# Performance work log

Hardware: AMD Instinct MI355X
Metric: run time of the kernel (lower is better)

## Reference

```python
import jax, jax.numpy as jnp
import numpy as np


def _conv3d(x, w, b, pad_t):
    # x: (b, c, t, h, w); w: (out_c, in_c, kt, 1, 1); conv only along time dim
    y = jax.lax.conv_general_dilated(
        x, w, window_strides=(1, 1, 1),
        padding=((pad_t, pad_t), (0, 0), (0, 0)),
        dimension_numbers=('NCDHW', 'OIDHW', 'NCDHW'))
    return y + b[None, :, None, None, None]


def setup_inputs() -> dict:
    key = jax.random.key(0)
    ks = jax.random.split(key, 8)
    b, t, c, h, w = 4, 16, 64, 96, 96
    cq = c // 8
    s = 0.05
    return {
        'x': jax.random.normal(ks[0], (b, t, c, h, w), jnp.float32),
        'wq': jax.random.normal(ks[1], (cq, c, 3, 1, 1), jnp.float32) * s,
        'bq': jax.random.normal(ks[2], (cq,), jnp.float32) * s,
        'wk': jax.random.normal(ks[3], (cq, c, 3, 1, 1), jnp.float32) * s,
        'bk': jax.random.normal(ks[4], (cq,), jnp.float32) * s,
        'wv': jax.random.normal(ks[5], (c, c, 1, 1, 1), jnp.float32) * s,
        'bv': jax.random.normal(ks[6], (c,), jnp.float32) * s,
        'gamma': jax.random.normal(ks[7], (1,), jnp.float32) * 0.1,
    }


def reference(x, wq, bq, wk, bk, wv, bv, gamma):
    b, t, c, h, w = x.shape
    xc = jnp.transpose(x, (0, 2, 1, 3, 4))  # (b, c, t, h, w)
    # q, k: (b, t, c//8 * h * w); v: (b, t, c * h * w)
    q = jnp.transpose(_conv3d(xc, wq, bq, 1), (0, 2, 1, 3, 4)).reshape(b, t, -1)
    k = jnp.transpose(_conv3d(xc, wk, bk, 1), (0, 2, 1, 3, 4)).reshape(b, t, -1)
    v = jnp.transpose(_conv3d(xc, wv, bv, 0), (0, 2, 1, 3, 4)).reshape(b, t, -1)
    energy = jnp.einsum('btd,bsd->bts', q, k)          # (b, t, t)
    heat = jax.nn.softmax(energy, axis=-1)             # softmax over dim 2
    out = jnp.einsum('bts,bsd->btd', heat, v).reshape(b, t, c, h, w)
    return gamma * out + x
```

## Files before the change

### kernel.cpp

```cpp
#include <hip/hip_runtime.h>
#include <math.h>

#define B_  4
#define T_  16
#define C_  64
#define CQ_ 8
#define HW_ 9216
#define NCH_ 576

typedef __attribute__((ext_vector_type(8))) short    s16x8;
typedef __attribute__((ext_vector_type(4))) float    f32x4;
typedef __attribute__((ext_vector_type(4))) unsigned u32x4;

static __device__ __forceinline__ short f2bf(float f) {
  union { float f; unsigned u; } v; v.f = f;
  return (short)((v.u + 0x7FFFu + ((v.u >> 16) & 1u)) >> 16);
}
static __device__ __forceinline__ unsigned pkbf(float lo, float hi) {
  unsigned r;
  asm("v_cvt_pk_bf16_f32 %0, %1, %2" : "=v"(r) : "v"(lo), "v"(hi));
  return r;
}
static __device__ __forceinline__ float ubf(unsigned u) {
  union { unsigned u; float f; } v; v.u = u; return v.f;
}

__global__ __launch_bounds__(256)
void k_prep(const float* __restrict__ wq, const float* __restrict__ wk,
            const float* __restrict__ wv, short* __restrict__ wqkb,
            short* __restrict__ wvb) {
  for (int idx = threadIdx.x; idx < 3072; idx += 256) {
    int j = idx & 7, lane = (idx >> 3) & 63, ks = idx >> 9;
    int m = lane & 15, lq = lane >> 4;
    int ci = (ks & 1) * 32 + lq * 8 + j;
    int d  = ks >> 1;
    float wval = (m < 8) ? wq[(m * C_ + ci) * 3 + d]
                         : wk[((m - 8) * C_ + ci) * 3 + d];
    wqkb[idx] = f2bf(wval);
  }
  for (int idx = threadIdx.x; idx < 4096; idx += 256) {
    int j = idx & 7, lane = (idx >> 3) & 63, fr = idx >> 9;
    int ct = fr >> 1, ks = fr & 1;
    int c  = ct * 16 + (lane & 15);
    int ci = ks * 32 + (lane >> 4) * 8 + j;
    wvb[idx] = f2bf(wv[c * C_ + ci]);
  }
}

__global__ __launch_bounds__(512, 4)
void k_energy(const float* __restrict__ x, const short* __restrict__ wqkb,
              const float* __restrict__ bq, const float* __restrict__ bk,
              float* __restrict__ partE) {
  __shared__ __attribute__((aligned(16))) short sh[29440];
  __shared__ float Ered[1024];

  const int b    = blockIdx.y;
  const int hw0  = blockIdx.x * 16;
  const int tid  = threadIdx.x;
  const int lane = tid & 63, w = tid >> 6;
  const int l15  = lane & 15, lq = lane >> 4;
  const f32x4 fz = {0.f, 0.f, 0.f, 0.f};

  for (int i = tid; i < 1152; i += 512)
    ((unsigned*)sh)[(i < 576) ? i : (9216 + i)] = 0;

  s16x8 afr[6];
#pragma unroll
  for (int ks = 0; ks < 6; ++ks)
    afr[ks] = *(const s16x8*)&wqkb[(ks * 64 + lane) * 8];

  const float* bias = (lq < 2) ? bq : bk;
  const int cqb = (lq & 1) * 4;
  const float b0 = bias[cqb + 0], b1 = bias[cqb + 1];
  const float b2 = bias[cqb + 2], b3 = bias[cqb + 3];

  {
    const int q4 = tid & 3;
    const int cp = (tid >> 2) & 31;
    const int s0 = tid >> 7;
    const float* xb = x + (size_t)(b * T_ * C_ + 2 * cp) * HW_ + hw0 + 4 * q4;
#pragma unroll
    for (int it = 0; it < 4; ++it) {
      const int s = s0 * 4 + it;
      float4 v0 = *(const float4*)(xb + (size_t)(s * C_) * HW_);
      float4 v1 = *(const float4*)(xb + (size_t)(s * C_) * HW_ + HW_);
      const int off = ((cp >> 2) ^ ((s + 1) & 7)) * 8 + 2 * (cp & 3);
      const int rb  = (s + 1) * 16 + 4 * q4;
      *(unsigned*)&sh[(rb + 0) * 72 + off] = pkbf(v0.x, v1.x);
      *(unsigned*)&sh[(rb + 1) * 72 + off] = pkbf(v0.y, v1.y);
      *(unsigned*)&sh[(rb + 2) * 72 + off] = pkbf(v0.z, v1.z);
      *(unsigned*)&sh[(rb + 3) * 72 + off] = pkbf(v0.w, v1.w);
    }
  }
  __syncthreads();

#pragma unroll
  for (int gl = 0; gl < 2; ++gl) {
    const int g = w * 2 + gl;
    f32x4 a = fz;
#pragma unroll
    for (int ks = 0; ks < 6; ++ks) {
      const int d = ks >> 1;
      const int row = (l15 + d) * 16 + g;
      const int chunk = (((ks & 1) * 4 + lq) ^ ((l15 + d) & 7));
      s16x8 bf = *(const s16x8*)&sh[row * 72 + chunk * 8];
      a = __builtin_amdgcn_mfma_f32_16x16x32_bf16(afr[ks], bf, a, 0, 0, 0);
    }
    const float v0 = a[0] + b0, v1 = a[1] + b1;
    const float v2 = a[2] + b2, v3 = a[3] + b3;
    const unsigned h01 = pkbf(v0, v1), h23 = pkbf(v2, v3);
    const unsigned l01 = pkbf(v0 - ubf(h01 << 16), v1 - ubf(h01 & 0xffff0000u));
    const unsigned l23 = pkbf(v2 - ubf(h23 << 16), v3 - ubf(h23 & 0xffff0000u));
    short* pl = &sh[20736 + (lq >> 1) * 4352 + l15 * 136 + g * 8 + (lq & 1) * 4];
    uint2 hh; hh.x = h01; hh.y = h23;
    uint2 ll; ll.x = l01; ll.y = l23;
    *(uint2*)pl          = hh;
    *(uint2*)(pl + 2176) = ll;
  }
  __syncthreads();

  if (w < 4) {
    const int off = l15 * 136 + w * 32 + lq * 8;
    const short* Qp = &sh[20736];
    const short* Kp = &sh[20736 + 4352];
    s16x8 qh = *(const s16x8*)&Qp[off];
    s16x8 ql = *(const s16x8*)&Qp[off + 2176];
    s16x8 kh = *(const s16x8*)&Kp[off];
    s16x8 kl = *(const s16x8*)&Kp[off + 2176];
    f32x4 e = fz;
    e = __builtin_amdgcn_mfma_f32_16x16x32_bf16(qh, kh, e, 0, 0, 0);
    e = __builtin_amdgcn_mfma_f32_16x16x32_bf16(qh, kl, e, 0, 0, 0);
    e = __builtin_amdgcn_mfma_f32_16x16x32_bf16(ql, kh, e, 0, 0, 0);
#pragma unroll
    for (int r = 0; r < 4; ++r)
      Ered[w * 256 + (lq * 4 + r) * 16 + l15] = e[r];
  }
  __syncthreads();

  if (tid < 256) {
    float e = Ered[tid] + Ered[256 + tid] + Ered[512 + tid] + Ered[768 + tid];
    partE[((size_t)(b * NCH_ + blockIdx.x)) * 256 + tid] = e;
  }
}

__global__ __launch_bounds__(256)
void k_softmax(const float* __restrict__ partE, float* __restrict__ heat) {
  const int b = blockIdx.x;
  const int tid = threadIdx.x;
  float e = 0.f;
  for (int ch = 0; ch < NCH_; ++ch)
    e += partE[((size_t)(b * NCH_ + ch)) * 256 + tid];
  float mx = e;
#pragma unroll
  for (int m = 1; m < 16; m <<= 1) mx = fmaxf(mx, __shfl_xor(mx, m, 64));
  float ex = expf(e - mx);
  float sm = ex;
#pragma unroll
  for (int m = 1; m < 16; m <<= 1) sm += __shfl_xor(sm, m, 64);
  heat[b * 256 + tid] = ex / sm;
}

__global__ __launch_bounds__(256, 3)
void k_mix(const float* __restrict__ x, const float* __restrict__ heat,
           const short* __restrict__ wvb, const float* __restrict__ bv,
           const float* __restrict__ gam, float* __restrict__ out) {
  __shared__ __attribute__((aligned(16))) short sm[20480];

  const int b    = blockIdx.y;
  const int hw0  = blockIdx.x * 16;
  const int tid  = threadIdx.x;
  const int lane = tid & 63;
  const int w    = tid >> 6;
  const int l15  = lane & 15;
  const int lq   = lane >> 4;

  union U8 { s16x8 v; int i[4]; unsigned u[4]; };
  const f32x4 fz = {0.f, 0.f, 0.f, 0.f};

  U8 ha; ha.i[0] = ha.i[1] = ha.i[2] = ha.i[3] = 0;
  if (lane < 32) {
    const float* hp = heat + b * 256 + l15 * 16 + lq * 8;
    float4 h0 = *(const float4*)hp;
    float4 h1 = *(const float4*)(hp + 4);
    ha.u[0] = pkbf(h0.x, h0.y); ha.u[1] = pkbf(h0.z, h0.w);
    ha.u[2] = pkbf(h1.x, h1.y); ha.u[3] = pkbf(h1.z, h1.w);
  }

  {
    const int ci = tid >> 2, q = tid & 3;
    const int sx = ci & 7;
    const float* xp = x + ((size_t)b * T_ * C_ + ci) * HW_ + hw0 + q * 4;
    short* r0 = &sm[(ci * 16 + q * 4) * 20];
#pragma unroll
    for (int P = 0; P < 8; ++P) {
      float4 v0 = *(const float4*)(xp + (size_t)(2 * P) * C_ * HW_);
      float4 v1 = *(const float4*)(xp + (size_t)(2 * P + 1) * C_ * HW_);
      const int ip = (P ^ sx) * 2;
      *(unsigned*)&r0[ip]      = pkbf(v0.x, v1.x);
      *(unsigned*)&r0[20 + ip] = pkbf(v0.y, v1.y);
      *(unsigned*)&r0[40 + ip] = pkbf(v0.z, v1.z);
      *(unsigned*)&r0[60 + ip] = pkbf(v0.w, v1.w);
    }
  }

  U8 a2[8];
#pragma unroll
  for (int fr = 0; fr < 8; ++fr)
    a2[fr].v = *(const s16x8*)&wvb[(fr * 64 + lane) * 8];

  asm volatile("s_waitcnt lgkmcnt(0)" ::: "memory");

  const int lq2 = lq & 1;
  f32x4 c1[16];
#pragma unroll
  for (int i = 0; i < 16; ++i) {
    const int ci = w * 16 + i;
    const short* row = &sm[(ci * 16 + l15) * 20];
    const int base = (lq2 * 4) ^ (i & 4);
    int2 D0 = *(const int2*)&row[2 * base];
    int2 D1 = *(const int2*)&row[2 * base + 4];
    U8 bx;
    const int t3 = i & 3;
    bx.i[0] = (t3 == 0) ? D0.x : (t3 == 1) ? D0.y : (t3 == 2) ? D1.x : D1.y;
    bx.i[1] = (t3 == 0) ? D0.y : (t3 == 1) ? D0.x : (t3 == 2) ? D1.y : D1.x;
    bx.i[2] = (t3 == 0) ? D1.x : (t3 == 1) ? D1.y : (t3 == 2) ? D0.x : D0.y;
    bx.i[3] = (t3 == 0) ? D1.y : (t3 == 1) ? D1.x : (t3 == 2) ? D0.y : D0.x;
    c1[i] = __builtin_amdgcn_mfma_f32_16x16x32_bf16(ha.v, bx.v, fz, 0, 0, 0);
  }
  __syncthreads();

  unsigned rc[32];
#pragma unroll
  for (int ct = 0; ct < 4; ++ct)
#pragma unroll
    for (int r = 0; r < 4; ++r) {
      const int c = ct * 16 + lq * 4 + r;
      const short* row = &sm[(c * 16 + l15) * 20];
      const int base = 4 * ((w >> 1) ^ (lq & 1)) + 2 * ((w & 1) ^ (r >> 1));
      int2 D = *(const int2*)&row[2 * base];
      rc[(ct * 4 + r) * 2 + 0] = (r & 1) ? (unsigned)D.y : (unsigned)D.x;
      rc[(ct * 4 + r) * 2 + 1] = (r & 1) ? (unsigned)D.x : (unsigned)D.y;
    }
  __syncthreads();

#pragma unroll
  for (int r = 0; r < 4; ++r) {
    const int t = lq * 4 + r;
    short* dst = &sm[(t * 16 + l15) * 72 + w * 16];
    u32x4 p0, p1;
    p0[0] = pkbf(c1[0][r],  c1[1][r]);  p0[1] = pkbf(c1[2][r],  c1[3][r]);
    p0[2] = pkbf(c1[4][r],  c1[5][r]);  p0[3] = pkbf(c1[6][r],  c1[7][r]);
    p1[0] = pkbf(c1[8][r],  c1[9][r]);  p1[1] = pkbf(c1[10][r], c1[11][r]);
    p1[2] = pkbf(c1[12][r], c1[13][r]); p1[3] = pkbf(c1[14][r], c1[15][r]);
    *(u32x4*)dst       = p0;
    *(u32x4*)(dst + 8) = p1;
  }

  f32x4 bvr[4];
#pragma unroll
  for (int ct = 0; ct < 4; ++ct)
    bvr[ct] = *(const f32x4*)(bv + ct * 16 + lq * 4);
  const float gamma = gam[0];
  __syncthreads();

#pragma unroll
  for (int ntq = 0; ntq < 4; ++ntq) {
    const int t = w * 4 + ntq;
    const short* xr0 = &sm[(t * 16 + l15) * 72];
    s16x8 b0 = *(const s16x8*)(xr0 + lq * 8);
    s16x8 b1 = *(const s16x8*)(xr0 + 32 + lq * 8);
    float* op = out + ((size_t)(b * T_ + t) * C_) * HW_ + hw0 + l15;
    const int half = ntq >> 1, odd = ntq & 1;
#pragma unroll
    for (int ct = 0; ct < 4; ++ct) {
      f32x4 acc = __builtin_amdgcn_mfma_f32_16x16x32_bf16(a2[ct * 2 + 0].v, b0, fz, 0, 0, 0);
      acc = __builtin_amdgcn_mfma_f32_16x16x32_bf16(a2[ct * 2 + 1].v, b1, acc, 0, 0, 0);
      const int cb = ct * 16 + lq * 4;
#pragma unroll
      for (int r = 0; r < 4; ++r) {
        const unsigned v = rc[(ct * 4 + r) * 2 + half];
        union { unsigned u; float f; } z;
        z.u = odd ? (v & 0xffff0000u) : (v << 16);
        __builtin_nontemporal_store(
            gamma * (acc[r] + bvr[ct][r]) + z.f,
            &op[(size_t)(cb + r) * HW_]);
      }
    }
  }
}

extern "C" void kernel_launch(void* const* d_in, const int* in_sizes, int n_in,
                              void* d_out, int out_size, void* d_ws, size_t ws_size,
                              hipStream_t stream) {
  const float* x   = (const float*)d_in[0];
  const float* wq  = (const float*)d_in[1];
  const float* bq  = (const float*)d_in[2];
  const float* wk  = (const float*)d_in[3];
  const float* bk  = (const float*)d_in[4];
  const float* wv  = (const float*)d_in[5];
  const float* bv  = (const float*)d_in[6];
  const float* gam = (const float*)d_in[7];
  float* out = (float*)d_out;

  short* wqkb  = (short*)d_ws;
  short* wvb   = wqkb + 3072;
  float* partE = (float*)(wvb + 4096 + 1024);
  float* heat  = partE + (size_t)B_ * NCH_ * 256;

  k_prep   <<<1, 256, 0, stream>>>(wq, wk, wv, wqkb, wvb);
  k_energy <<<dim3(NCH_, B_), 512, 0, stream>>>(x, wqkb, bq, bk, partE);
  k_softmax<<<dim3(B_),       256, 0, stream>>>(partE, heat);
  k_mix    <<<dim3(HW_ / 16, B_), 256, 0, stream>>>(x, heat, wvb, bv, gam, out);
}
```

Baseline: 148.2 us.

## Widen softmax reduction to 1024 threads and double k_mix tile to 32 pixels

The softmax kernel now splits the 576-chunk partial-energy sum across four thread groups and combines them through shared memory, which shortens the serial reduction loop per thread. The mix kernel now handles 32 spatial positions per block with 512 threads (two 16-pixel halves across eight waves), doubling shared memory and halving the grid. This is meant to amortize weight and heat loads and per-block overhead. The cost is fewer blocks and higher LDS use per block, which may reduce occupancy.

```diff
diff --git a/kernel.cpp b/kernel.cpp
--- a/kernel.cpp
+++ b/kernel.cpp
@@ -143,34 +143,43 @@
   }
 }
 
-__global__ __launch_bounds__(256)
+__global__ __launch_bounds__(1024)
 void k_softmax(const float* __restrict__ partE, float* __restrict__ heat) {
+  __shared__ float red[1024];
   const int b = blockIdx.x;
   const int tid = threadIdx.x;
-  float e = 0.f;
-  for (int ch = 0; ch < NCH_; ++ch)
-    e += partE[((size_t)(b * NCH_ + ch)) * 256 + tid];
-  float mx = e;
-#pragma unroll
-  for (int m = 1; m < 16; m <<= 1) mx = fmaxf(mx, __shfl_xor(mx, m, 64));
-  float ex = expf(e - mx);
-  float sm = ex;
-#pragma unroll
-  for (int m = 1; m < 16; m <<= 1) sm += __shfl_xor(sm, m, 64);
-  heat[b * 256 + tid] = ex / sm;
-}
-
-__global__ __launch_bounds__(256, 3)
+  const int e = tid & 255, z = tid >> 8;
+  float s = 0.f;
+  for (int ch = z; ch < NCH_; ch += 4)
+    s += partE[((size_t)(b * NCH_ + ch)) * 256 + e];
+  red[tid] = s;
+  __syncthreads();
+  if (z == 0) {
+    float ev = red[e] + red[256 + e] + red[512 + e] + red[768 + e];
+    float mx = ev;
+#pragma unroll
+    for (int m = 1; m < 16; m <<= 1) mx = fmaxf(mx, __shfl_xor(mx, m, 64));
+    float ex = expf(ev - mx);
+    float sm = ex;
+#pragma unroll
+    for (int m = 1; m < 16; m <<= 1) sm += __shfl_xor(sm, m, 64);
+    heat[b * 256 + e] = ex / sm;
+  }
+}
+
+__global__ __launch_bounds__(512, 2)
 void k_mix(const float* __restrict__ x, const float* __restrict__ heat,
            const short* __restrict__ wvb, const float* __restrict__ bv,
            const float* __restrict__ gam, float* __restrict__ out) {
-  __shared__ __attribute__((aligned(16))) short sm[20480];
+  __shared__ __attribute__((aligned(16))) short sm[40960];
 
   const int b    = blockIdx.y;
-  const int hw0  = blockIdx.x * 16;
+  const int hw0  = blockIdx.x * 32;
   const int tid  = threadIdx.x;
   const int lane = tid & 63;
   const int w    = tid >> 6;
+  const int wg   = w & 3;
+  const int gh   = w >> 2;
   const int l15  = lane & 15;
   const int lq   = lane >> 4;
 
@@ -187,10 +196,11 @@
   }
 
   {
-    const int ci = tid >> 2, q = tid & 3;
-    const int sx = ci & 7;
-    const float* xp = x + ((size_t)b * T_ * C_ + ci) * HW_ + hw0 + q * 4;
-    short* r0 = &sm[(ci * 16 + q * 4) * 20];
+    const int ciS = wg * 16 + (lane >> 2);
+    const int gS  = gh * 16 + (lane & 3) * 4;
+    const int sx  = ciS & 7;
+    const float* xp = x + ((size_t)b * T_ * C_ + ciS) * HW_ + hw0 + gS;
+    short* r0 = &sm[(ciS * 32 + gS) * 20];
 #pragma unroll
     for (int P = 0; P < 8; ++P) {
       float4 v0 = *(const float4*)(xp + (size_t)(2 * P) * C_ * HW_);
@@ -214,8 +224,8 @@
   f32x4 c1[16];
 #pragma unroll
   for (int i = 0; i < 16; ++i) {
-    const int ci = w * 16 + i;
-    const short* row = &sm[(ci * 16 + l15) * 20];
+    const int ci = wg * 16 + i;
+    const short* row = &sm[(ci * 32 + gh * 16 + l15) * 20];
     const int base = (lq2 * 4) ^ (i & 4);
     int2 D0 = *(const int2*)&row[2 * base];
     int2 D1 = *(const int2*)&row[2 * base + 4];
@@ -235,8 +245,8 @@
 #pragma unroll
     for (int r = 0; r < 4; ++r) {
       const int c = ct * 16 + lq * 4 + r;
-      const short* row = &sm[(c * 16 + l15) * 20];
-      const int base = 4 * ((w >> 1) ^ (lq & 1)) + 2 * ((w & 1) ^ (r >> 1));
+      const short* row = &sm[(c * 32 + gh * 16 + l15) * 20];
+      const int base = 4 * ((wg >> 1) ^ (lq & 1)) + 2 * ((wg & 1) ^ (r >> 1));
       int2 D = *(const int2*)&row[2 * base];
       rc[(ct * 4 + r) * 2 + 0] = (r & 1) ? (unsigned)D.y : (unsigned)D.x;
       rc[(ct * 4 + r) * 2 + 1] = (r & 1) ? (unsigned)D.x : (unsigned)D.y;
@@ -246,7 +256,7 @@
 #pragma unroll
   for (int r = 0; r < 4; ++r) {
     const int t = lq * 4 + r;
-    short* dst = &sm[(t * 16 + l15) * 72 + w * 16];
+    short* dst = &sm[(t * 32 + gh * 16 + l15) * 72 + wg * 16];
     u32x4 p0, p1;
     p0[0] = pkbf(c1[0][r],  c1[1][r]);  p0[1] = pkbf(c1[2][r],  c1[3][r]);
     p0[2] = pkbf(c1[4][r],  c1[5][r]);  p0[3] = pkbf(c1[6][r],  c1[7][r]);
@@ -265,11 +275,11 @@
 
 #pragma unroll
   for (int ntq = 0; ntq < 4; ++ntq) {
-    const int t = w * 4 + ntq;
-    const short* xr0 = &sm[(t * 16 + l15) * 72];
+    const int t = wg * 4 + ntq;
+    const short* xr0 = &sm[(t * 32 + gh * 16 + l15) * 72];
     s16x8 b0 = *(const s16x8*)(xr0 + lq * 8);
     s16x8 b1 = *(const s16x8*)(xr0 + 32 + lq * 8);
-    float* op = out + ((size_t)(b * T_ + t) * C_) * HW_ + hw0 + l15;
+    float* op = out + ((size_t)(b * T_ + t) * C_) * HW_ + hw0 + gh * 16 + l15;
     const int half = ntq >> 1, odd = ntq & 1;
 #pragma unroll
     for (int ct = 0; ct < 4; ++ct) {
@@ -309,6 +319,6 @@
 
   k_prep   <<<1, 256, 0, stream>>>(wq, wk, wv, wqkb, wvb);
   k_energy <<<dim3(NCH_, B_), 512, 0, stream>>>(x, wqkb, bq, bk, partE);
-  k_softmax<<<dim3(B_),       256, 0, stream>>>(partE, heat);
-  k_mix    <<<dim3(HW_ / 16, B_), 256, 0, stream>>>(x, heat, wvb, bv, gam, out);
-}
+  k_softmax<<<dim3(B_),      1024, 0, stream>>>(partE, heat);
+  k_mix    <<<dim3(HW_ / 32, B_), 512, 0, stream>>>(x, heat, wvb, bv, gam, out);
+}
```

Result: slower. 159.3 us (+7.5%).

## Process two spatial tiles per energy block with register prefetch; parallelize softmax reduction

Applied to the files above, without the earlier changes.

Each k_energy block now handles two 16-pixel tiles, issuing the global loads for the second tile into registers while the first tile's MFMA work runs, then staging them into shared memory after a barrier. This halves the grid and overlaps memory latency with compute, but raises register pressure (occupancy hint lowered to 2) and adds more barriers per block. k_softmax now uses 1024 threads to split the 576-chunk partial-energy reduction four ways, with a final reduction through shared memory.

```diff
diff --git a/kernel.cpp b/kernel.cpp
--- a/kernel.cpp
+++ b/kernel.cpp
@@ -47,7 +47,7 @@
   }
 }
 
-__global__ __launch_bounds__(512, 4)
+__global__ __launch_bounds__(512, 2)
 void k_energy(const float* __restrict__ x, const short* __restrict__ wqkb,
               const float* __restrict__ bq, const float* __restrict__ bk,
               float* __restrict__ partE) {
@@ -55,7 +55,7 @@
   __shared__ float Ered[1024];
 
   const int b    = blockIdx.y;
-  const int hw0  = blockIdx.x * 16;
+  const int hw0  = blockIdx.x * 32;
   const int tid  = threadIdx.x;
   const int lane = tid & 63, w = tid >> 6;
   const int l15  = lane & 15, lq = lane >> 4;
@@ -74,25 +74,33 @@
   const float b0 = bias[cqb + 0], b1 = bias[cqb + 1];
   const float b2 = bias[cqb + 2], b3 = bias[cqb + 3];
 
-  {
-    const int q4 = tid & 3;
-    const int cp = (tid >> 2) & 31;
-    const int s0 = tid >> 7;
-    const float* xb = x + (size_t)(b * T_ * C_ + 2 * cp) * HW_ + hw0 + 4 * q4;
-#pragma unroll
-    for (int it = 0; it < 4; ++it) {
-      const int s = s0 * 4 + it;
-      float4 v0 = *(const float4*)(xb + (size_t)(s * C_) * HW_);
-      float4 v1 = *(const float4*)(xb + (size_t)(s * C_) * HW_ + HW_);
-      const int off = ((cp >> 2) ^ ((s + 1) & 7)) * 8 + 2 * (cp & 3);
-      const int rb  = (s + 1) * 16 + 4 * q4;
-      *(unsigned*)&sh[(rb + 0) * 72 + off] = pkbf(v0.x, v1.x);
-      *(unsigned*)&sh[(rb + 1) * 72 + off] = pkbf(v0.y, v1.y);
-      *(unsigned*)&sh[(rb + 2) * 72 + off] = pkbf(v0.z, v1.z);
-      *(unsigned*)&sh[(rb + 3) * 72 + off] = pkbf(v0.w, v1.w);
-    }
-  }
-  __syncthreads();
+  const int q4 = tid & 3;
+  const int cp = (tid >> 2) & 31;
+  const int s0 = tid >> 7;
+  const int offb = 2 * (cp & 3);
+  const float* xb = x + (size_t)(b * T_ * C_ + 2 * cp) * HW_ + hw0 + 4 * q4;
+
+#pragma unroll
+  for (int it = 0; it < 4; ++it) {
+    const int s = s0 * 4 + it;
+    float4 v0 = *(const float4*)(xb + (size_t)(s * C_) * HW_);
+    float4 v1 = *(const float4*)(xb + (size_t)(s * C_) * HW_ + HW_);
+    const int off = ((cp >> 2) ^ ((s + 1) & 7)) * 8 + offb;
+    const int rb  = (s + 1) * 16 + 4 * q4;
+    *(unsigned*)&sh[(rb + 0) * 72 + off] = pkbf(v0.x, v1.x);
+    *(unsigned*)&sh[(rb + 1) * 72 + off] = pkbf(v0.y, v1.y);
+    *(unsigned*)&sh[(rb + 2) * 72 + off] = pkbf(v0.z, v1.z);
+    *(unsigned*)&sh[(rb + 3) * 72 + off] = pkbf(v0.w, v1.w);
+  }
+  __syncthreads();
+
+  float4 p0[4], p1[4];
+#pragma unroll
+  for (int it = 0; it < 4; ++it) {
+    const int s = s0 * 4 + it;
+    p0[it] = *(const float4*)(xb + (size_t)(s * C_) * HW_ + 16);
+    p1[it] = *(const float4*)(xb + (size_t)(s * C_) * HW_ + HW_ + 16);
+  }
 
 #pragma unroll
   for (int gl = 0; gl < 2; ++gl) {
@@ -119,6 +127,16 @@
   }
   __syncthreads();
 
+#pragma unroll
+  for (int it = 0; it < 4; ++it) {
+    const int s = s0 * 4 + it;
+    const int off = ((cp >> 2) ^ ((s + 1) & 7)) * 8 + offb;
+    const int rb  = (s + 1) * 16 + 4 * q4;
+    *(unsigned*)&sh[(rb + 0) * 72 + off] = pkbf(p0[it].x, p1[it].x);
+    *(unsigned*)&sh[(rb + 1) * 72 + off] = pkbf(p0[it].y, p1[it].y);
+    *(unsigned*)&sh[(rb + 2) * 72 + off] = pkbf(p0[it].z, p1[it].z);
+    *(unsigned*)&sh[(rb + 3) * 72 + off] = pkbf(p0[it].w, p1[it].w);
+  }
   if (w < 4) {
     const int off = l15 * 136 + w * 32 + lq * 8;
     const short* Qp = &sh[20736];
@@ -139,25 +157,79 @@
 
   if (tid < 256) {
     float e = Ered[tid] + Ered[256 + tid] + Ered[512 + tid] + Ered[768 + tid];
-    partE[((size_t)(b * NCH_ + blockIdx.x)) * 256 + tid] = e;
-  }
-}
-
-__global__ __launch_bounds__(256)
+    partE[((size_t)(b * NCH_ + 2 * blockIdx.x)) * 256 + tid] = e;
+  }
+#pragma unroll
+  for (int gl = 0; gl < 2; ++gl) {
+    const int g = w * 2 + gl;
+    f32x4 a = fz;
+#pragma unroll
+    for (int ks = 0; ks < 6; ++ks) {
+      const int d = ks >> 1;
+      const int row = (l15 + d) * 16 + g;
+      const int chunk = (((ks & 1) * 4 + lq) ^ ((l15 + d) & 7));
+      s16x8 bf = *(const s16x8*)&sh[row * 72 + chunk * 8];
+      a = __builtin_amdgcn_mfma_f32_16x16x32_bf16(afr[ks], bf, a, 0, 0, 0);
+    }
+    const float v0 = a[0] + b0, v1 = a[1] + b1;
+    const float v2 = a[2] + b2, v3 = a[3] + b3;
+    const unsigned h01 = pkbf(v0, v1), h23 = pkbf(v2, v3);
+    const unsigned l01 = pkbf(v0 - ubf(h01 << 16), v1 - ubf(h01 & 0xffff0000u));
+    const unsigned l23 = pkbf(v2 - ubf(h23 << 16), v3 - ubf(h23 & 0xffff0000u));
+    short* pl = &sh[20736 + (lq >> 1) * 4352 + l15 * 136 + g * 8 + (lq & 1) * 4];
+    uint2 hh; hh.x = h01; hh.y = h23;
+    uint2 ll; ll.x = l01; ll.y = l23;
+    *(uint2*)pl          = hh;
+    *(uint2*)(pl + 2176) = ll;
+  }
+  __syncthreads();
+
+  if (w < 4) {
+    const int off = l15 * 136 + w * 32 + lq * 8;
+    const short* Qp = &sh[20736];
+    const short* Kp = &sh[20736 + 4352];
+    s16x8 qh = *(const s16x8*)&Qp[off];
+    s16x8 ql = *(const s16x8*)&Qp[off + 2176];
+    s16x8 kh = *(const s16x8*)&Kp[off];
+    s16x8 kl = *(const s16x8*)&Kp[off + 2176];
+    f32x4 e = fz;
+    e = __builtin_amdgcn_mfma_f32_16x16x32_bf16(qh, kh, e, 0, 0, 0);
+    e = __builtin_amdgcn_mfma_f32_16x16x32_bf16(qh, kl, e, 0, 0, 0);
+    e = __builtin_amdgcn_mfma_f32_16x16x32_bf16(ql, kh, e, 0, 0, 0);
+#pragma unroll
+    for (int r = 0; r < 4; ++r)
+      Ered[w * 256 + (lq * 4 + r) * 16 + l15] = e[r];
+  }
+  __syncthreads();
+
+  if (tid < 256) {
+    float e = Ered[tid] + Ered[256 + tid] + Ered[512 + tid] + Ered[768 + tid];
+    partE[((size_t)(b * NCH_ + 2 * blockIdx.x + 1)) * 256 + tid] = e;
+  }
+}
+
+__global__ __launch_bounds__(1024)
 void k_softmax(const float* __restrict__ partE, float* __restrict__ heat) {
+  __shared__ float red[1024];
   const int b = blockIdx.x;
   const int tid = threadIdx.x;
-  float e = 0.f;
-  for (int ch = 0; ch < NCH_; ++ch)
-    e += partE[((size_t)(b * NCH_ + ch)) * 256 + tid];
-  float mx = e;
-#pragma unroll
-  for (int m = 1; m < 16; m <<= 1) mx = fmaxf(mx, __shfl_xor(mx, m, 64));
-  float ex = expf(e - mx);
-  float sm = ex;
-#pragma unroll
-  for (int m = 1; m < 16; m <<= 1) sm += __shfl_xor(sm, m, 64);
-  heat[b * 256 + tid] = ex / sm;
+  const int e = tid & 255, z = tid >> 8;
+  float s = 0.f;
+  for (int ch = z; ch < NCH_; ch += 4)
+    s += partE[((size_t)(b * NCH_ + ch)) * 256 + e];
+  red[tid] = s;
+  __syncthreads();
+  if (z == 0) {
+    float ev = red[e] + red[256 + e] + red[512 + e] + red[768 + e];
+    float mx = ev;
+#pragma unroll
+    for (int m = 1; m < 16; m <<= 1) mx = fmaxf(mx, __shfl_xor(mx, m, 64));
+    float ex = expf(ev - mx);
+    float sm = ex;
+#pragma unroll
+    for (int m = 1; m < 16; m <<= 1) sm += __shfl_xor(sm, m, 64);
+    heat[b * 256 + e] = ex / sm;
+  }
 }
 
 __global__ __launch_bounds__(256, 3)
@@ -308,7 +380,7 @@
   float* heat  = partE + (size_t)B_ * NCH_ * 256;
 
   k_prep   <<<1, 256, 0, stream>>>(wq, wk, wv, wqkb, wvb);
-  k_energy <<<dim3(NCH_, B_), 512, 0, stream>>>(x, wqkb, bq, bk, partE);
-  k_softmax<<<dim3(B_),       256, 0, stream>>>(partE, heat);
+  k_energy <<<dim3(NCH_ / 2, B_), 512, 0, stream>>>(x, wqkb, bq, bk, partE);
+  k_softmax<<<dim3(B_),          1024, 0, stream>>>(partE, heat);
   k_mix    <<<dim3(HW_ / 16, B_), 256, 0, stream>>>(x, heat, wvb, bv, gam, out);
 }
```

New measurement: 163.1 us. 1.1x slower.
